# Kernel optimization log

Measured on AMD Instinct MI355X. Metric: run time of the kernel, lower is better.

The kernel has to match this reference:

```python
import jax, jax.numpy as jnp
import numpy as np

DIM = 64
WIDTH = 128
INPUT_DIM = 16
N_NODES = 50000
N_EDGES = 100000
N_GRAPHS = 2500
STEPS = 5


def setup_inputs() -> dict:
    key = jax.random.key(0)
    ks = jax.random.split(key, 24)
    d = DIM
    def nrm(i, shape, fan_in):
        return jax.random.normal(ks[i], shape, jnp.float32) / np.float32(np.sqrt(fan_in))
    return {
        "x": jax.random.normal(ks[0], (N_NODES, INPUT_DIM - 1), jnp.float32),
        "z": jax.random.normal(ks[1], (N_NODES,), jnp.float32),
        "edge_attr": jax.random.uniform(ks[2], (N_EDGES, 5), jnp.float32),
        "lin0_w": nrm(3, (INPUT_DIM, d), INPUT_DIM),
        "lin0_b": jnp.zeros((d,), jnp.float32),
        "emlp_w1": nrm(4, (5, WIDTH), 5),
        "emlp_b1": jnp.zeros((WIDTH,), jnp.float32),
        "emlp_w2": nrm(5, (WIDTH, d * d), WIDTH),
        "emlp_b2": jnp.zeros((d * d,), jnp.float32),
        "conv_root": nrm(6, (d, d), d),
        "conv_bias": jnp.zeros((d,), jnp.float32),
        "gru_wi": nrm(7, (3 * d, d), d),
        "gru_wh": nrm(8, (3 * d, d), d),
        "gru_bi": jnp.zeros((3 * d,), jnp.float32),
        "gru_bh": jnp.zeros((3 * d,), jnp.float32),
        "lstm_wi": nrm(9, (4 * d, 2 * d), 2 * d),
        "lstm_wh": nrm(10, (4 * d, d), d),
        "lstm_bi": jnp.zeros((4 * d,), jnp.float32),
        "lstm_bh": jnp.zeros((4 * d,), jnp.float32),
        "lin1_w": nrm(11, (2 * d, d), 2 * d),
        "lin1_b": jnp.zeros((d,), jnp.float32),
        "lin2_w": nrm(12, (d, 1), d),
        "lin2_b": jnp.zeros((1,), jnp.float32),
        "edge_index": jax.random.randint(ks[13], (2, N_EDGES), 0, N_NODES),
        "batch": jnp.sort(jax.random.randint(ks[14], (N_NODES,), 0, N_GRAPHS)),
        "num_graphs": N_GRAPHS,
    }


def reference(x, z, edge_attr, lin0_w, lin0_b, emlp_w1, emlp_b1, emlp_w2, emlp_b2,
              conv_root, conv_bias, gru_wi, gru_wh, gru_bi, gru_bh,
              lstm_wi, lstm_wh, lstm_bi, lstm_bh, lin1_w, lin1_b, lin2_w, lin2_b,
              edge_index, batch, num_graphs):
    d = lin0_w.shape[1]
    n = x.shape[0]
    src, dst = edge_index[0], edge_index[1]
    # lin0 on [x | z]
    out = jax.nn.relu(jnp.concatenate([x, z[:, None]], axis=-1) @ lin0_w + lin0_b)  # [N, d]
    h = out
    # edge MLP -> per-edge weight matrix [E, d, d] (edge_attr fixed, compute once)
    ew = (jax.nn.relu(edge_attr @ emlp_w1 + emlp_b1) @ emlp_w2 + emlp_b2).reshape(-1, d, d)
    deg = jax.ops.segment_sum(jnp.ones_like(src, jnp.float32), dst, num_segments=n)
    denom = jnp.maximum(deg, 1.0)[:, None]
    for _ in range(STEPS):
        # NNConv: gather-matmul-scatter(mean) + root transform + bias
        msg = jnp.einsum('ei,eio->eo', out[src], ew)  # [E, d]
        aggr = jax.ops.segment_sum(msg, dst, num_segments=n) / denom
        m = jax.nn.relu(aggr + out @ conv_root + conv_bias)
        # GRU cell (torch gate order r, z, n)
        gi = m @ gru_wi.T + gru_bi
        gh = h @ gru_wh.T + gru_bh
        i_r, i_z, i_n = jnp.split(gi, 3, axis=-1)
        h_r, h_z, h_n = jnp.split(gh, 3, axis=-1)
        r = jax.nn.sigmoid(i_r + h_r)
        zg = jax.nn.sigmoid(i_z + h_z)
        ng = jnp.tanh(i_n + r * h_n)
        h = (1.0 - zg) * ng + zg * h
        out = h
    # Set2Set pooling (LSTM(2d -> d), torch gate order i, f, g, o)
    B = num_graphs
    q_star = jnp.zeros((B, 2 * d), out.dtype)
    hh = jnp.zeros((B, d), out.dtype)
    cc = jnp.zeros((B, d), out.dtype)
    for _ in range(STEPS):
        g = q_star @ lstm_wi.T + lstm_bi + hh @ lstm_wh.T + lstm_bh
        gi_, gf_, gg_, go_ = jnp.split(g, 4, axis=-1)
        cc = jax.nn.sigmoid(gf_) * cc + jax.nn.sigmoid(gi_) * jnp.tanh(gg_)
        hh = jax.nn.sigmoid(go_) * jnp.tanh(cc)
        q = hh
        e = jnp.sum(out * q[batch], axis=-1)  # [N]
        emax = jax.ops.segment_max(e, batch, num_segments=B)
        a = jnp.exp(e - emax[batch])
        asum = jax.ops.segment_sum(a, batch, num_segments=B) + 1e-16
        a = a / asum[batch]
        r_pool = jax.ops.segment_sum(a[:, None] * out, batch, num_segments=B)  # [B, d]
        q_star = jnp.concatenate([q, r_pool], axis=-1)
    y = jax.nn.relu(q_star @ lin1_w + lin1_b) @ lin2_w + lin2_b
    return y.reshape(-1)
```

## Files before the change

kernel.cpp:

```cpp
#include <hip/hip_runtime.h>
#include <hip/hip_bf16.h>

#define NN 50000
#define NE 100000
#define NG 2500
#define WW 128
#define EPAD 100096
#define KCH 264

typedef _Float16 h8 __attribute__((ext_vector_type(8)));
typedef _Float16 h4 __attribute__((ext_vector_type(4)));
typedef float    f4 __attribute__((ext_vector_type(4)));

#define GLOAD_LDS16(g, l) __builtin_amdgcn_global_load_lds( \
    (const __attribute__((address_space(1))) void*)(g),     \
    (__attribute__((address_space(3))) void*)(l), 16, 0, 0)

__device__ __forceinline__ float sigf(float x) { return 1.0f / (1.0f + __expf(-x)); }

__global__ void k_zero4(float4* __restrict__ p, int n4) {
    int i = blockIdx.x * 256 + threadIdx.x;
    if (i < n4) p[i] = make_float4(0.f, 0.f, 0.f, 0.f);
}

__global__ void k_transpose(float* dst, const float* src, int rows, int cols) {
    int idx = blockIdx.x * 256 + threadIdx.x;
    if (idx >= rows * cols) return;
    int r = idx / cols, c = idx % cols;
    dst[c * rows + r] = src[idx];
}

__global__ void k_lin0(const float* __restrict__ x, const float* __restrict__ z,
                       const float* __restrict__ w, const float* __restrict__ b,
                       float* __restrict__ s) {
    int idx = blockIdx.x * 256 + threadIdx.x;
    int n = idx >> 6, o = idx & 63;
    float acc = b[o];
#pragma unroll
    for (int i = 0; i < 15; i++) acc += x[n * 15 + i] * w[i * 64 + o];
    acc += z[n] * w[15 * 64 + o];
    s[idx] = fmaxf(acc, 0.0f);
}

__global__ void k_deg(const int* __restrict__ dstI, float* __restrict__ deg) {
    int e = blockIdx.x * 256 + threadIdx.x;
    if (e < NE) atomicAdd(&deg[dstI[e]], 1.0f);
}

__global__ void k_s16(const float* __restrict__ s, _Float16* __restrict__ s16) {
    int i = blockIdx.x * 256 + threadIdx.x;
    float4 v = ((const float4*)s)[i];
    h4 o = { (_Float16)v.x, (_Float16)v.y, (_Float16)v.z, (_Float16)v.w };
    *((h4*)s16 + i) = o;
}

__global__ void k_gstart(const int* __restrict__ batch, int* __restrict__ gstart) {
    int n = blockIdx.x * 256 + threadIdx.x;
    if (n > NN) return;
    int b1 = (n < NN) ? batch[n] : NG;
    int b0 = (n == 0) ? -1 : batch[n - 1];
    for (int g = b0 + 1; g <= b1; g++) gstart[g] = n;
}

__global__ void k_emlp_t(const float* __restrict__ ea, const float* __restrict__ w1,
                         const float* __restrict__ b1, _Float16* __restrict__ hidT) {
    __shared__ _Float16 hl[132][64];
    int t = threadIdx.x;
    int e0 = blockIdx.x * 64;
    int e_l = t & 63, w = t >> 6;
    int e = e0 + e_l;
    float a0 = 0, a1 = 0, a2 = 0, a3 = 0, a4 = 0;
    if (e < NE) {
        a0 = ea[e * 5 + 0]; a1 = ea[e * 5 + 1]; a2 = ea[e * 5 + 2];
        a3 = ea[e * 5 + 3]; a4 = ea[e * 5 + 4];
    }
    for (int h = w * 32; h < w * 32 + 32; h++) {
        float acc = b1[h];
        acc += a0 * w1[0 * 128 + h] + a1 * w1[1 * 128 + h] + a2 * w1[2 * 128 + h]
             + a3 * w1[3 * 128 + h] + a4 * w1[4 * 128 + h];
        hl[h][e_l] = (_Float16)fmaxf(acc, 0.0f);
    }
    if (t < 64) hl[128][t] = (_Float16)1.0f;
    else if (t < 128) hl[129][t - 64] = (_Float16)0.0f;
    else if (t < 192) hl[130][t - 128] = (_Float16)0.0f;
    else hl[131][t - 192] = (_Float16)0.0f;
    __syncthreads();
#pragma unroll
    for (int it = 0; it < 33; it++) {
        int idx = it * 256 + t;
        int h = idx >> 6, el = idx & 63;
        hidT[(size_t)h * EPAD + e0 + el] = hl[h][el];
    }
}

__global__ void k_prep_B(const float* __restrict__ w2, const float* __restrict__ b2,
                         _Float16* __restrict__ Bp) {
    int g = blockIdx.x * 256 + threadIdx.x;
    int l = g & 63, tt = (g >> 6) & 3, c = g >> 8;
    int n = tt * 16 + (l & 15);
    int kb = c * 32 + (l >> 4) * 8;
    h8 v;
#pragma unroll
    for (int j = 0; j < 8; j++) {
        int k = kb + j;
        float f = 0.0f;
        if (k < 8192) f = w2[(size_t)k * 64 + n];
        else if (k < 8256) f = b2[(k - 8192) * 64 + n];
        v[j] = (_Float16)f;
    }
    *((h8*)Bp + g) = v;
}

__global__ void k_prep_W(const float* __restrict__ conv_root,
                         const float* __restrict__ gru_wi,
                         const float* __restrict__ gru_wh,
                         _Float16* __restrict__ Bw) {
    int g = blockIdx.x * 256 + threadIdx.x;
    if (g >= 56 * 64) return;
    int l = g & 63, unit = g >> 6;
    int kb = ((unit & 1) * 32) + (l >> 4) * 8;
    h8 v;
    if (unit < 8) {
        int nt = unit >> 1;
        int n = nt * 16 + (l & 15);
#pragma unroll
        for (int j = 0; j < 8; j++) v[j] = (_Float16)conv_root[(kb + j) * 64 + n];
    } else if (unit < 32) {
        int nt = (unit - 8) >> 1;
        int o = nt * 16 + (l & 15);
#pragma unroll
        for (int j = 0; j < 8; j++) v[j] = (_Float16)gru_wi[o * 64 + kb + j];
    } else {
        int nt = (unit - 32) >> 1;
        int o = nt * 16 + (l & 15);
#pragma unroll
        for (int j = 0; j < 8; j++) v[j] = (_Float16)gru_wh[o * 64 + kb + j];
    }
    *((h8*)Bw + g) = v;
}

__global__ __launch_bounds__(128, 2) void k_fused(
        const _Float16* __restrict__ s16, const _Float16* __restrict__ hidT,
        const _Float16* __restrict__ Bp, const int* __restrict__ srcI,
        const int* __restrict__ dstI, float* __restrict__ aggr) {
    __shared__ uint4 Bl[2048];
    __shared__ _Float16 hle[128][4];
    int t = threadIdx.x, w = t >> 6, lane = t & 63;
    int m = lane & 15, q = lane >> 4;
    int e_blk = blockIdx.x * 128;
    int ew0 = e_blk + w * 64;

    h8 sA[4][2];
#pragma unroll
    for (int mt = 0; mt < 4; mt++) {
        int e = ew0 + mt * 16 + m;
        int src = (e < NE) ? srcI[e] : 0;
        const _Float16* sp = s16 + (size_t)src * 64;
        sA[mt][0] = *(const h8*)(sp + q * 8);
        sA[mt][1] = *(const h8*)(sp + 32 + q * 8);
    }
    f4 acc[4][4];
#pragma unroll
    for (int mt = 0; mt < 4; mt++)
#pragma unroll
        for (int nt = 0; nt < 4; nt++) acc[mt][nt] = (f4){0.f, 0.f, 0.f, 0.f};

    for (int sc = 0; sc < 33; sc++) {
        __syncthreads();
        const uint4* bsrc = (const uint4*)Bp + (size_t)sc * 2048;
#pragma unroll
        for (int r = 0; r < 16; r++) {
            int idx = r * 128 + t;
            GLOAD_LDS16(bsrc + idx, Bl + idx);
        }
        {
            const _Float16* hp = hidT + (size_t)(sc * 4) * EPAD + e_blk + t;
            h4 hv4;
            hv4[0] = hp[0];
            hv4[1] = hp[EPAD];
            hv4[2] = hp[2 * (size_t)EPAD];
            hv4[3] = hp[3 * (size_t)EPAD];
            *(h4*)&hle[t][0] = hv4;
        }
        __syncthreads();
        h4 hf[4];
#pragma unroll
        for (int mt = 0; mt < 4; mt++)
            hf[mt] = *(const h4*)&hle[w * 64 + mt * 16 + m][0];
#pragma unroll
        for (int cc = 0; cc < 8; cc++) {
            h8 b0 = *(const h8*)&Bl[(cc * 4 + 0) * 64 + lane];
            h8 b1 = *(const h8*)&Bl[(cc * 4 + 1) * 64 + lane];
            h8 b2 = *(const h8*)&Bl[(cc * 4 + 2) * 64 + lane];
            h8 b3 = *(const h8*)&Bl[(cc * 4 + 3) * 64 + lane];
            int hi = cc >> 1, kh = cc & 1;
#pragma unroll
            for (int mt = 0; mt < 4; mt++) {
                h8 a = sA[mt][kh] * hf[mt][hi];
                acc[mt][0] = __builtin_amdgcn_mfma_f32_16x16x32_f16(a, b0, acc[mt][0], 0, 0, 0);
                acc[mt][1] = __builtin_amdgcn_mfma_f32_16x16x32_f16(a, b1, acc[mt][1], 0, 0, 0);
                acc[mt][2] = __builtin_amdgcn_mfma_f32_16x16x32_f16(a, b2, acc[mt][2], 0, 0, 0);
                acc[mt][3] = __builtin_amdgcn_mfma_f32_16x16x32_f16(a, b3, acc[mt][3], 0, 0, 0);
            }
        }
    }
#pragma unroll
    for (int mt = 0; mt < 4; mt++) {
        int eb = ew0 + mt * 16 + q * 4;
#pragma unroll
        for (int r = 0; r < 4; r++) {
            int e = eb + r;
            if (e < NE) {
                int d = dstI[e];
                float* ap = aggr + (size_t)d * 64 + m;
                atomicAdd(ap + 0,  acc[mt][0][r]);
                atomicAdd(ap + 16, acc[mt][1][r]);
                atomicAdd(ap + 32, acc[mt][2][r]);
                atomicAdd(ap + 48, acc[mt][3][r]);
            }
        }
    }
}

__global__ __launch_bounds__(256) void k_combine2(
        float* __restrict__ s, _Float16* __restrict__ s16,
        const float* __restrict__ aggr, const float* __restrict__ deg,
        const _Float16* __restrict__ Bw, const float* __restrict__ cb,
        const float* __restrict__ bi, const float* __restrict__ bh) {
    __shared__ _Float16 ml[4][16][72];
    int t = threadIdx.x, w = t >> 6, lane = t & 63;
    int m = lane & 15, q = lane >> 4;
    int nb = blockIdx.x * 64 + w * 16;

    h8 sa0, sa1;
    {
        int node = nb + m; if (node >= NN) node = NN - 1;
        const _Float16* sp = s16 + (size_t)node * 64;
        sa0 = *(const h8*)(sp + q * 8);
        sa1 = *(const h8*)(sp + 32 + q * 8);
    }
    const h8* BW = (const h8*)Bw;

    f4 X[4], GH[12];
#pragma unroll
    for (int nt = 0; nt < 4; nt++) {
        X[nt] = (f4){0.f, 0.f, 0.f, 0.f};
        X[nt] = __builtin_amdgcn_mfma_f32_16x16x32_f16(sa0, BW[(nt * 2 + 0) * 64 + lane], X[nt], 0, 0, 0);
        X[nt] = __builtin_amdgcn_mfma_f32_16x16x32_f16(sa1, BW[(nt * 2 + 1) * 64 + lane], X[nt], 0, 0, 0);
    }
#pragma unroll
    for (int nt = 0; nt < 12; nt++) {
        GH[nt] = (f4){0.f, 0.f, 0.f, 0.f};
        GH[nt] = __builtin_amdgcn_mfma_f32_16x16x32_f16(sa0, BW[(32 + nt * 2 + 0) * 64 + lane], GH[nt], 0, 0, 0);
        GH[nt] = __builtin_amdgcn_mfma_f32_16x16x32_f16(sa1, BW[(32 + nt * 2 + 1) * 64 + lane], GH[nt], 0, 0, 0);
    }
#pragma unroll
    for (int r = 0; r < 4; r++) {
        int node = nb + q * 4 + r; if (node >= NN) node = NN - 1;
        float dn = fmaxf(deg[node], 1.0f);
#pragma unroll
        for (int nt = 0; nt < 4; nt++) {
            int o = nt * 16 + m;
            float mv = X[nt][r] + aggr[(size_t)node * 64 + o] / dn + cb[o];
            ml[w][q * 4 + r][o] = (_Float16)fmaxf(mv, 0.0f);
        }
    }
    __syncthreads();
    h8 ma0 = *(const h8*)&ml[w][m][q * 8];
    h8 ma1 = *(const h8*)&ml[w][m][32 + q * 8];

    f4 GI[12];
#pragma unroll
    for (int nt = 0; nt < 12; nt++) {
        GI[nt] = (f4){0.f, 0.f, 0.f, 0.f};
        GI[nt] = __builtin_amdgcn_mfma_f32_16x16x32_f16(ma0, BW[(8 + nt * 2 + 0) * 64 + lane], GI[nt], 0, 0, 0);
        GI[nt] = __builtin_amdgcn_mfma_f32_16x16x32_f16(ma1, BW[(8 + nt * 2 + 1) * 64 + lane], GI[nt], 0, 0, 0);
    }
#pragma unroll
    for (int og = 0; og < 4; og++) {
        int o = og * 16 + m;
        float bir = bi[o],       bhr = bh[o];
        float biz = bi[64 + o],  bhz = bh[64 + o];
        float bin = bi[128 + o], bhn = bh[128 + o];
#pragma unroll
        for (int r = 0; r < 4; r++) {
            int node = nb + q * 4 + r;
            if (node >= NN) continue;
            float rr = sigf(GI[og][r] + bir + GH[og][r] + bhr);
            float zz = sigf(GI[4 + og][r] + biz + GH[4 + og][r] + bhz);
            float ng = tanhf(GI[8 + og][r] + bin + rr * (GH[8 + og][r] + bhn));
            float hold = s[(size_t)node * 64 + o];
            float hnew = (1.0f - zz) * ng + zz * hold;
            s[(size_t)node * 64 + o] = hnew;
            s16[(size_t)node * 64 + o] = (_Float16)hnew;
        }
    }
}

__global__ void k_s2s(float* __restrict__ q_star, float* __restrict__ hh,
                      float* __restrict__ cc, const float* __restrict__ LiT,
                      const float* __restrict__ LhT, const float* __restrict__ bi,
                      const float* __restrict__ bh, const float* __restrict__ s,
                      const int* __restrict__ gstart, float* __restrict__ e_v) {
    __shared__ float qs[128], hv[64], g[256], qn[64];
    int b = blockIdx.x, t = threadIdx.x;
    if (t < 128) qs[t] = q_star[b * 128 + t];
    else if (t < 192) hv[t - 128] = hh[b * 64 + t - 128];
    __syncthreads();
    float acc = bi[t] + bh[t];
    for (int k = 0; k < 128; k++) acc += qs[k] * LiT[k * 256 + t];
    for (int k = 0; k < 64; k++) acc += hv[k] * LhT[k * 256 + t];
    g[t] = acc;
    __syncthreads();
    if (t < 64) {
        float c_new = sigf(g[64 + t]) * cc[b * 64 + t] + sigf(g[t]) * tanhf(g[128 + t]);
        cc[b * 64 + t] = c_new;
        float hq = sigf(g[192 + t]) * tanhf(c_new);
        hh[b * 64 + t] = hq;
        qn[t] = hq;
        q_star[b * 128 + t] = hq;
    }
    __syncthreads();
    if (t >= 64) return;
    int o = t;
    int n0 = gstart[b], n1 = gstart[b + 1];
    float q = qn[o];
    float mx = -3.4e38f;
    for (int n = n0; n < n1; n++) {
        float v = s[(size_t)n * 64 + o] * q;
#pragma unroll
        for (int off = 32; off; off >>= 1) v += __shfl_xor(v, off, 64);
        if (o == 0) e_v[n] = v;
        mx = fmaxf(mx, v);
    }
    float asum = 0.0f, rp = 0.0f;
    for (int n = n0; n < n1; n++) {
        float a = __expf(e_v[n] - mx);
        asum += a;
        rp += a * s[(size_t)n * 64 + o];
    }
    q_star[b * 128 + 64 + o] = rp / (asum + 1e-16f);
}

__global__ void k_final(const float* __restrict__ q_star, const float* __restrict__ w1,
                        const float* __restrict__ b1, const float* __restrict__ w2,
                        const float* __restrict__ b2, float* __restrict__ y) {
    __shared__ float qs[128];
    int b = blockIdx.x, t = threadIdx.x;
    qs[t] = q_star[b * 128 + t];
    qs[64 + t] = q_star[b * 128 + 64 + t];
    __syncthreads();
    float acc = b1[t];
    for (int k = 0; k < 128; k++) acc += qs[k] * w1[k * 64 + t];
    float hid = fmaxf(acc, 0.0f) * w2[t];
#pragma unroll
    for (int off = 32; off; off >>= 1) hid += __shfl_down(hid, off, 64);
    if (t == 0) y[b] = hid + b2[0];
}

static inline void zero_f(float* p, size_t nfloats, hipStream_t stream) {
    int n4 = (int)(nfloats / 4);
    k_zero4<<<(n4 + 255) / 256, 256, 0, stream>>>((float4*)p, n4);
}

extern "C" void kernel_launch(void* const* d_in, const int* in_sizes, int n_in,
                              void* d_out, int out_size, void* d_ws, size_t ws_size,
                              hipStream_t stream) {
    const float* x       = (const float*)d_in[0];
    const float* z       = (const float*)d_in[1];
    const float* ea      = (const float*)d_in[2];
    const float* lin0_w  = (const float*)d_in[3];
    const float* lin0_b  = (const float*)d_in[4];
    const float* emlp_w1 = (const float*)d_in[5];
    const float* emlp_b1 = (const float*)d_in[6];
    const float* emlp_w2 = (const float*)d_in[7];
    const float* emlp_b2 = (const float*)d_in[8];
    const float* conv_r  = (const float*)d_in[9];
    const float* conv_b  = (const float*)d_in[10];
    const float* gru_wi  = (const float*)d_in[11];
    const float* gru_wh  = (const float*)d_in[12];
    const float* gru_bi  = (const float*)d_in[13];
    const float* gru_bh  = (const float*)d_in[14];
    const float* lstm_wi = (const float*)d_in[15];
    const float* lstm_wh = (const float*)d_in[16];
    const float* lstm_bi = (const float*)d_in[17];
    const float* lstm_bh = (const float*)d_in[18];
    const float* lin1_w  = (const float*)d_in[19];
    const float* lin1_b  = (const float*)d_in[20];
    const float* lin2_w  = (const float*)d_in[21];
    const float* lin2_b  = (const float*)d_in[22];
    const int* eidx      = (const int*)d_in[23];
    const int* batch     = (const int*)d_in[24];
    const int* srcI = eidx;
    const int* dstI = eidx + NE;
    float* y = (float*)d_out;

    char* w = (char*)d_ws;
    size_t off = 0;
    auto alloc = [&](size_t bytes) -> void* {
        void* p = w + off;
        off += (bytes + 255) & ~(size_t)255;
        return p;
    };
    float* s      = (float*)alloc((size_t)NN * 64 * 4);
    float* aggr   = (float*)alloc((size_t)NN * 64 * 4);
    float* deg    = (float*)alloc((size_t)NN * 4);
    float* e_v    = (float*)alloc((size_t)NN * 4);
    float* q_star = (float*)alloc((size_t)NG * 128 * 4);
    float* hh     = (float*)alloc((size_t)NG * 64 * 4);
    float* cc     = (float*)alloc((size_t)NG * 64 * 4);
    float* LiT    = (float*)alloc(256 * 128 * 4);
    float* LhT    = (float*)alloc(256 * 64 * 4);
    int*   gstart = (int*)alloc((size_t)(NG + 1) * 4);
    _Float16* s16 = (_Float16*)alloc((size_t)NN * 64 * 2);
    _Float16* hidT= (_Float16*)alloc((size_t)132 * EPAD * 2);
    _Float16* Bp  = (_Float16*)alloc((size_t)KCH * 4 * 64 * 8 * 2);
    _Float16* Bw  = (_Float16*)alloc((size_t)56 * 64 * 8 * 2);
    (void)ws_size;

    k_transpose<<<(256 * 128 + 255) / 256, 256, 0, stream>>>(LiT, lstm_wi, 256, 128);
    k_transpose<<<(256 * 64 + 255) / 256, 256, 0, stream>>>(LhT, lstm_wh, 256, 64);
    k_prep_W<<<14, 256, 0, stream>>>(conv_r, gru_wi, gru_wh, Bw);

    k_lin0<<<NN * 64 / 256, 256, 0, stream>>>(x, z, lin0_w, lin0_b, s);
    k_s16<<<NN * 16 / 256, 256, 0, stream>>>(s, s16);
    zero_f(deg, NN, stream);
    k_deg<<<(NE + 255) / 256, 256, 0, stream>>>(dstI, deg);
    k_gstart<<<(NN + 256) / 256, 256, 0, stream>>>(batch, gstart);
    k_emlp_t<<<EPAD / 64, 256, 0, stream>>>(ea, emlp_w1, emlp_b1, hidT);
    k_prep_B<<<KCH * 4 * 64 / 256, 256, 0, stream>>>(emlp_w2, emlp_b2, Bp);

    for (int step = 0; step < 5; step++) {
        zero_f(aggr, (size_t)NN * 64, stream);
        k_fused<<<EPAD / 128, 128, 0, stream>>>(s16, hidT, Bp, srcI, dstI, aggr);
        k_combine2<<<(NN + 63) / 64, 256, 0, stream>>>(s, s16, aggr, deg, Bw,
                                                       conv_b, gru_bi, gru_bh);
    }

    zero_f(q_star, (size_t)NG * 128 + NG * 64 + NG * 64, stream);
    for (int it = 0; it < 5; it++) {
        k_s2s<<<NG, 256, 0, stream>>>(q_star, hh, cc, LiT, LhT, lstm_bi, lstm_bh,
                                      s, gstart, e_v);
    }
    k_final<<<NG, 64, 0, stream>>>(q_star, lin1_w, lin1_b, lin2_w, lin2_b, y);
}
```

Before: 1.062 ms.

## Double-buffer edge-MLP weight chunks and prefetch interleaved hidden activations in registers

The fused edge-conv kernel now double-buffers the per-chunk weight tile in LDS, issuing the next chunk's global-to-LDS loads before computing on the current one. The edge hidden activations are stored interleaved in groups of four, so each lane loads its four fp16 values with one vector load straight into registers. This removes the LDS staging buffer and one barrier per chunk. LDS use doubles and the launch-bounds occupancy hint is dropped, which may lower occupancy or change register allocation.

Result: slower. 1.289 ms (+21.4%).

```diff
diff --git a/kernel.cpp b/kernel.cpp
--- a/kernel.cpp
+++ b/kernel.cpp
@@ -63,7 +63,7 @@
 }
 
 __global__ void k_emlp_t(const float* __restrict__ ea, const float* __restrict__ w1,
-                         const float* __restrict__ b1, _Float16* __restrict__ hidT) {
+                         const float* __restrict__ b1, _Float16* __restrict__ hidT2) {
     __shared__ _Float16 hl[132][64];
     int t = threadIdx.x;
     int e0 = blockIdx.x * 64;
@@ -85,11 +85,11 @@
     else if (t < 192) hl[130][t - 128] = (_Float16)0.0f;
     else hl[131][t - 192] = (_Float16)0.0f;
     __syncthreads();
-#pragma unroll
-    for (int it = 0; it < 33; it++) {
-        int idx = it * 256 + t;
-        int h = idx >> 6, el = idx & 63;
-        hidT[(size_t)h * EPAD + e0 + el] = hl[h][el];
+    for (int idx = t; idx < 33 * 64; idx += 256) {
+        int j = idx >> 6, el = idx & 63;
+        h4 v = { hl[j * 4 + 0][el], hl[j * 4 + 1][el],
+                 hl[j * 4 + 2][el], hl[j * 4 + 3][el] };
+        *(h4*)(hidT2 + ((size_t)j * EPAD + e0 + el) * 4) = v;
     }
 }
 
@@ -139,12 +139,11 @@
     *((h8*)Bw + g) = v;
 }
 
-__global__ __launch_bounds__(128, 2) void k_fused(
-        const _Float16* __restrict__ s16, const _Float16* __restrict__ hidT,
+__global__ __launch_bounds__(128) void k_fused(
+        const _Float16* __restrict__ s16, const _Float16* __restrict__ hidT2,
         const _Float16* __restrict__ Bp, const int* __restrict__ srcI,
         const int* __restrict__ dstI, float* __restrict__ aggr) {
-    __shared__ uint4 Bl[2048];
-    __shared__ _Float16 hle[128][4];
+    __shared__ uint4 Bl[2][2048];
     int t = threadIdx.x, w = t >> 6, lane = t & 63;
     int m = lane & 15, q = lane >> 4;
     int e_blk = blockIdx.x * 128;
@@ -165,44 +164,55 @@
 #pragma unroll
         for (int nt = 0; nt < 4; nt++) acc[mt][nt] = (f4){0.f, 0.f, 0.f, 0.f};
 
-    for (int sc = 0; sc < 33; sc++) {
-        __syncthreads();
-        const uint4* bsrc = (const uint4*)Bp + (size_t)sc * 2048;
+    {
+        const uint4* bsrc = (const uint4*)Bp;
 #pragma unroll
         for (int r = 0; r < 16; r++) {
             int idx = r * 128 + t;
-            GLOAD_LDS16(bsrc + idx, Bl + idx);
-        }
-        {
-            const _Float16* hp = hidT + (size_t)(sc * 4) * EPAD + e_blk + t;
-            h4 hv4;
-            hv4[0] = hp[0];
-            hv4[1] = hp[EPAD];
-            hv4[2] = hp[2 * (size_t)EPAD];
-            hv4[3] = hp[3 * (size_t)EPAD];
-            *(h4*)&hle[t][0] = hv4;
-        }
+            GLOAD_LDS16(bsrc + idx, &Bl[0][idx]);
+        }
+    }
+    h4 hfc[4], hfn[4];
+#pragma unroll
+    for (int mt = 0; mt < 4; mt++) {
+        int e = ew0 + mt * 16 + m;
+        hfc[mt] = *(const h4*)(hidT2 + (size_t)e * 4);
+    }
+
+    for (int sc = 0; sc < 33; sc++) {
+        int cur = sc & 1;
         __syncthreads();
-        h4 hf[4];
-#pragma unroll
-        for (int mt = 0; mt < 4; mt++)
-            hf[mt] = *(const h4*)&hle[w * 64 + mt * 16 + m][0];
+        if (sc < 32) {
+            const uint4* bsrc = (const uint4*)Bp + (size_t)(sc + 1) * 2048;
+#pragma unroll
+            for (int r = 0; r < 16; r++) {
+                int idx = r * 128 + t;
+                GLOAD_LDS16(bsrc + idx, &Bl[1 - cur][idx]);
+            }
+#pragma unroll
+            for (int mt = 0; mt < 4; mt++) {
+                int e = ew0 + mt * 16 + m;
+                hfn[mt] = *(const h4*)(hidT2 + ((size_t)(sc + 1) * EPAD + e) * 4);
+            }
+        }
 #pragma unroll
         for (int cc = 0; cc < 8; cc++) {
-            h8 b0 = *(const h8*)&Bl[(cc * 4 + 0) * 64 + lane];
-            h8 b1 = *(const h8*)&Bl[(cc * 4 + 1) * 64 + lane];
-            h8 b2 = *(const h8*)&Bl[(cc * 4 + 2) * 64 + lane];
-            h8 b3 = *(const h8*)&Bl[(cc * 4 + 3) * 64 + lane];
+            h8 b0 = *(const h8*)&Bl[cur][(cc * 4 + 0) * 64 + lane];
+            h8 b1 = *(const h8*)&Bl[cur][(cc * 4 + 1) * 64 + lane];
+            h8 b2 = *(const h8*)&Bl[cur][(cc * 4 + 2) * 64 + lane];
+            h8 b3 = *(const h8*)&Bl[cur][(cc * 4 + 3) * 64 + lane];
             int hi = cc >> 1, kh = cc & 1;
 #pragma unroll
             for (int mt = 0; mt < 4; mt++) {
-                h8 a = sA[mt][kh] * hf[mt][hi];
+                h8 a = sA[mt][kh] * hfc[mt][hi];
                 acc[mt][0] = __builtin_amdgcn_mfma_f32_16x16x32_f16(a, b0, acc[mt][0], 0, 0, 0);
                 acc[mt][1] = __builtin_amdgcn_mfma_f32_16x16x32_f16(a, b1, acc[mt][1], 0, 0, 0);
                 acc[mt][2] = __builtin_amdgcn_mfma_f32_16x16x32_f16(a, b2, acc[mt][2], 0, 0, 0);
                 acc[mt][3] = __builtin_amdgcn_mfma_f32_16x16x32_f16(a, b3, acc[mt][3], 0, 0, 0);
             }
         }
+#pragma unroll
+        for (int mt = 0; mt < 4; mt++) hfc[mt] = hfn[mt];
     }
 #pragma unroll
     for (int mt = 0; mt < 4; mt++) {
@@ -413,7 +423,7 @@
     float* LhT    = (float*)alloc(256 * 64 * 4);
     int*   gstart = (int*)alloc((size_t)(NG + 1) * 4);
     _Float16* s16 = (_Float16*)alloc((size_t)NN * 64 * 2);
-    _Float16* hidT= (_Float16*)alloc((size_t)132 * EPAD * 2);
+    _Float16* hidT2 = (_Float16*)alloc((size_t)33 * EPAD * 4 * 2);
     _Float16* Bp  = (_Float16*)alloc((size_t)KCH * 4 * 64 * 8 * 2);
     _Float16* Bw  = (_Float16*)alloc((size_t)56 * 64 * 8 * 2);
     (void)ws_size;
@@ -427,12 +437,12 @@
     zero_f(deg, NN, stream);
     k_deg<<<(NE + 255) / 256, 256, 0, stream>>>(dstI, deg);
     k_gstart<<<(NN + 256) / 256, 256, 0, stream>>>(batch, gstart);
-    k_emlp_t<<<EPAD / 64, 256, 0, stream>>>(ea, emlp_w1, emlp_b1, hidT);
+    k_emlp_t<<<EPAD / 64, 256, 0, stream>>>(ea, emlp_w1, emlp_b1, hidT2);
     k_prep_B<<<KCH * 4 * 64 / 256, 256, 0, stream>>>(emlp_w2, emlp_b2, Bp);
 
     for (int step = 0; step < 5; step++) {
         zero_f(aggr, (size_t)NN * 64, stream);
-        k_fused<<<EPAD / 128, 128, 0, stream>>>(s16, hidT, Bp, srcI, dstI, aggr);
+        k_fused<<<EPAD / 128, 128, 0, stream>>>(s16, hidT2, Bp, srcI, dstI, aggr);
         k_combine2<<<(NN + 63) / 64, 256, 0, stream>>>(s, s16, aggr, deg, Bw,
                                                        conv_b, gru_bi, gru_bh);
     }
```
